# Optimization experiments

Measured on AMD Instinct MI355X. Metric: run time of the kernel, lower is better.

## Reference

```python
import jax, jax.numpy as jnp
import numpy as np
import math

B, S, H = 8, 1024, 1024
LN_EPS = 1e-5  # assumed epsilon of create_normalization_layer('layer_norm')


def setup_inputs() -> dict:
    key = jax.random.key(0)
    ks = jax.random.split(key, 6)
    context = jax.random.normal(ks[0], (B, S, H), dtype=jnp.float32)
    mask = jnp.ones((B, 1, S), dtype=jnp.int32)
    prior = jax.random.uniform(ks[1], (B, S, S), dtype=jnp.float32)
    # LayerNorm params
    gamma = jnp.ones((H,), dtype=jnp.float32)
    beta = jnp.zeros((H,), dtype=jnp.float32)
    # Dense projections (Glorot-like init)
    scale = 1.0 / np.sqrt(H)
    Wk = jax.random.normal(ks[2], (H, H), dtype=jnp.float32) * scale
    bk = jnp.zeros((H,), dtype=jnp.float32)
    Wq = jax.random.normal(ks[3], (H, H), dtype=jnp.float32) * scale
    bq = jnp.zeros((H,), dtype=jnp.float32)
    return {"context": context, "mask": mask, "prior": prior,
            "gamma": gamma, "beta": beta, "Wk": Wk, "bk": bk, "Wq": Wq, "bq": bq}


def reference(context, mask, prior, gamma, beta, Wk, bk, Wq, bq):
    dtype = context.dtype
    s = context.shape[1]
    hs = context.shape[2]
    i = jnp.arange(s)
    adj_upper = i[:, None] == (i[None, :] - 1)          # [S,S] superdiagonal
    adj_lower = i[:, None] == (i[None, :] + 1)          # subdiagonal
    adj_mask = adj_upper | adj_lower
    pad = mask[:, 0, :].astype(bool)                    # [B,S]
    pad2d = pad[:, :, None] & pad[:, None, :]           # [B,S,S]
    final_adj = adj_mask[None, :, :] & pad2d

    # LayerNorm over last axis
    mu = jnp.mean(context, axis=-1, keepdims=True)
    var = jnp.mean(jnp.square(context - mu), axis=-1, keepdims=True)
    cn = (context - mu) * jax.lax.rsqrt(var + LN_EPS) * gamma + beta

    k = cn @ Wk + bk                                    # [B,S,H]
    q = cn @ Wq + bq
    scores = jnp.einsum('bsh,bth->bst', q, k) / math.sqrt(hs)
    scores = jnp.where(final_adj, scores, jnp.asarray(-1e9, dtype))
    neibor = jax.nn.softmax(scores, axis=-1)
    neibor = jnp.sqrt(neibor * jnp.swapaxes(neibor, 1, 2) + 1e-9)
    neibor = prior + (1.0 - prior) * neibor

    triu = i[None, :] >= i[:, None]                     # [S,S] upper incl diag
    tri = triu.astype(dtype)
    b_eye = jnp.eye(s, dtype=bool)

    t = jnp.log(neibor + 1e-9)
    t = jnp.where(adj_upper[None, :, :], t, jnp.asarray(0.0, dtype))
    t = jnp.einsum('bij,jk->bik', t, tri)               # cumulative over cols
    g = jnp.exp(jnp.einsum('ij,bjk->bik', tri, t))      # hierarchical prefix product
    keep = jnp.logical_not(jnp.logical_xor(triu, b_eye))
    g = jnp.where(keep[None, :, :], g, jnp.asarray(0.0, dtype))
    neibor_diag = jnp.where(b_eye[None, :, :], jnp.asarray(1e-9, dtype), neibor)
    g = g + jnp.swapaxes(g, 1, 2) + neibor_diag
    g = g / (jnp.sum(g, axis=-1, keepdims=True) + 1e-9)

    f2d = pad2d.astype(dtype)
    g = g * f2d
    neibor = neibor * f2d
    return g, neibor
```

## Files before the change

### kernel.cpp

```cpp
#include <hip/hip_runtime.h>
#include <hip/hip_bf16.h>

#define SB 8
#define SS 1024
#define SH 1024
#define LN_EPS 1e-5f

typedef unsigned short u16;
typedef __attribute__((ext_vector_type(8))) short bf16x8;
typedef __attribute__((ext_vector_type(4))) float f32x4;

__device__ __forceinline__ u16 f2bf(float f) {
  __hip_bfloat16 h = __float2bfloat16(f);
  return *reinterpret_cast<u16*>(&h);
}
__device__ __forceinline__ float bf2f(u16 x) {
  unsigned v = ((unsigned)x) << 16;
  return __builtin_bit_cast(float, v);
}

__device__ __forceinline__ void gld16(const void* g, void* l) {
  __builtin_amdgcn_global_load_lds(
      (const __attribute__((address_space(1))) void*)g,
      (__attribute__((address_space(3))) void*)l, 16, 0, 0);
}

__global__ __launch_bounds__(256) void ln_cast(const float* __restrict__ x,
                                               const float* __restrict__ gamma,
                                               const float* __restrict__ beta,
                                               u16* __restrict__ cnb) {
  const int r = blockIdx.x;
  const int t = threadIdx.x;
  const int wave = t >> 6, lane = t & 63;
  const float* xr = x + (size_t)r * SH;
  float4 v = *(const float4*)(xr + 4 * t);

  __shared__ float p1[4], p2[4];
  float s = v.x + v.y + v.z + v.w;
#pragma unroll
  for (int off = 32; off > 0; off >>= 1) s += __shfl_down(s, off, 64);
  if (lane == 0) p1[wave] = s;
  __syncthreads();
  const float mu = (p1[0] + p1[1] + p1[2] + p1[3]) * (1.0f / SH);

  float d0 = v.x - mu, d1 = v.y - mu, d2 = v.z - mu, d3 = v.w - mu;
  float ss = d0 * d0 + d1 * d1 + d2 * d2 + d3 * d3;
#pragma unroll
  for (int off = 32; off > 0; off >>= 1) ss += __shfl_down(ss, off, 64);
  if (lane == 0) p2[wave] = ss;
  __syncthreads();
  const float rstd = rsqrtf((p2[0] + p2[1] + p2[2] + p2[3]) * (1.0f / SH) + LN_EPS);

  float4 gm = *(const float4*)(gamma + 4 * t);
  float4 bt = *(const float4*)(beta + 4 * t);
  ushort4 o;
  o.x = f2bf(d0 * rstd * gm.x + bt.x);
  o.y = f2bf(d1 * rstd * gm.y + bt.y);
  o.z = f2bf(d2 * rstd * gm.z + bt.z);
  o.w = f2bf(d3 * rstd * gm.w + bt.w);
  *(ushort4*)(cnb + (size_t)r * SH + 4 * t) = o;
}

__global__ __launch_bounds__(256) void wcast(const float* __restrict__ Wq,
                                             const float* __restrict__ Wk,
                                             u16* __restrict__ Wq_bf,
                                             u16* __restrict__ Wk_bf) {
  const size_t e = ((size_t)blockIdx.x * 256 + threadIdx.x) * 4;
  const size_t M = (size_t)SH * SH;
  const float* src;
  u16* dst;
  if (e < M) { src = Wq + e; dst = Wq_bf + e; }
  else       { src = Wk + (e - M); dst = Wk_bf + (e - M); }
  float4 v = *(const float4*)src;
  ushort4 o;
  o.x = f2bf(v.x); o.y = f2bf(v.y); o.z = f2bf(v.z); o.w = f2bf(v.w);
  *(ushort4*)dst = o;
}

__global__ __launch_bounds__(256) void wkbq_kernel(const float* __restrict__ Wk,
                                                   const float* __restrict__ bq,
                                                   float* __restrict__ wkbq) {
  const int wave = threadIdx.x >> 6, lane = threadIdx.x & 63;
  const int h = blockIdx.x * 4 + wave;
  const float* row = Wk + (size_t)h * SH;
  float s = 0.f;
#pragma unroll
  for (int v = 0; v < 4; ++v) {
    const int j = v * 256 + lane * 4;
    float4 w = *(const float4*)(row + j);
    float4 b = *(const float4*)(bq + j);
    s += w.x * b.x + w.y * b.y + w.z * b.z + w.w * b.w;
  }
#pragma unroll
  for (int off = 32; off > 0; off >>= 1) s += __shfl_down(s, off, 64);
  if (lane == 0) wkbq[h] = s;
}

#define BM 128
#define BN 128
#define BK 32

template <int GKv, int GNv, bool BF16OUT>
__global__ __launch_bounds__(256) void gemm_bt_t(const u16* __restrict__ A,
                                                 const u16* __restrict__ Bt,
                                                 void* __restrict__ Cv) {
  __shared__ u16 As[BM * BK];
  __shared__ u16 Bs[BN * BK];
  const int tid = threadIdx.x;
  const int m0 = blockIdx.y * BM;
  const int n0 = blockIdx.x * BN;
  const int wave = tid >> 6, lane = tid & 63;
  const int wm = (wave & 1) * 64, wn = (wave >> 1) * 64;
  const int l15 = lane & 15, q = lane >> 4;

  f32x4 acc[4][4] = {};

  const int srow = tid >> 2;
  const int scol = 8 * (tid & 3);
  const u16* gA = A + (size_t)(m0 + srow) * GKv + scol;
  const u16* gB = Bt + (size_t)(n0 + srow) * GKv + scol;
  u16* lA = &As[srow * BK + scol];
  u16* lB = &Bs[srow * BK + scol];

  for (int k0 = 0; k0 < GKv; k0 += BK) {
    __syncthreads();
    gld16(gA + k0, lA);
    gld16(gA + (size_t)64 * GKv + k0, lA + 64 * BK);
    gld16(gB + k0, lB);
    gld16(gB + (size_t)64 * GKv + k0, lB + 64 * BK);
    __syncthreads();

    bf16x8 af[4], bfr[4];
#pragma unroll
    for (int fm = 0; fm < 4; ++fm)
      af[fm] = *(const bf16x8*)&As[(wm + fm * 16 + l15) * BK + q * 8];
#pragma unroll
    for (int fn = 0; fn < 4; ++fn)
      bfr[fn] = *(const bf16x8*)&Bs[(wn + fn * 16 + l15) * BK + q * 8];
#pragma unroll
    for (int fm = 0; fm < 4; ++fm)
#pragma unroll
      for (int fn = 0; fn < 4; ++fn)
        acc[fm][fn] = __builtin_amdgcn_mfma_f32_16x16x32_bf16(
            af[fm], bfr[fn], acc[fm][fn], 0, 0, 0);
  }

#pragma unroll
  for (int fm = 0; fm < 4; ++fm)
#pragma unroll
    for (int fn = 0; fn < 4; ++fn) {
      const int row0 = m0 + wm + fm * 16 + q * 4;
      const int col = n0 + wn + fn * 16 + l15;
#pragma unroll
      for (int r = 0; r < 4; ++r) {
        const size_t idx = (size_t)(row0 + r) * GNv + col;
        if (BF16OUT) ((u16*)Cv)[idx] = f2bf(acc[fm][fn][r]);
        else ((float*)Cv)[idx] = acc[fm][fn][r];
      }
    }
}

__global__ __launch_bounds__(256) void adj_dots(const float* __restrict__ U,
                                                const u16* __restrict__ cnb,
                                                const float* __restrict__ wkbq,
                                                float* __restrict__ pup,
                                                float* __restrict__ pdn) {
  const int wave = threadIdx.x >> 6;
  const int lane = threadIdx.x & 63;
  const int r = blockIdx.x * 4 + wave;
  const int s = r & (SS - 1);
  const bool has_up = (s < SS - 1), has_dn = (s > 0);
  const float* ur = U + (size_t)r * SH;
  const u16* up = cnb + (size_t)(has_up ? r + 1 : r) * SH;
  const u16* dn = cnb + (size_t)(has_dn ? r - 1 : r) * SH;

  float du = 0.f, dd = 0.f;
#pragma unroll
  for (int v = 0; v < 4; ++v) {
    const int j = v * 256 + lane * 4;
    float4 uv = *(const float4*)(ur + j);
    float4 wv = *(const float4*)(wkbq + j);
    ushort4 us = *(const ushort4*)(up + j);
    ushort4 ds = *(const ushort4*)(dn + j);
    const float t0 = uv.x + wv.x, t1 = uv.y + wv.y;
    const float t2 = uv.z + wv.z, t3 = uv.w + wv.w;
    du += bf2f(us.x) * t0 + bf2f(us.y) * t1 + bf2f(us.z) * t2 + bf2f(us.w) * t3;
    dd += bf2f(ds.x) * t0 + bf2f(ds.y) * t1 + bf2f(ds.z) * t2 + bf2f(ds.w) * t3;
  }
#pragma unroll
  for (int off = 32; off > 0; off >>= 1) {
    du += __shfl_down(du, off, 64);
    dd += __shfl_down(dd, off, 64);
  }
  if (lane == 0) {
    const float scale = 0.03125f;
    du *= scale;
    dd *= scale;
    float pu, pd;
    if (!has_dn) { pu = 1.f; pd = 0.f; }
    else if (!has_up) { pu = 0.f; pd = 1.f; }
    else {
      const float m = fmaxf(du, dd);
      const float eu = __expf(du - m), ed = __expf(dd - m);
      const float inv = 1.f / (eu + ed);
      pu = eu * inv;
      pd = ed * inv;
    }
    pup[r] = pu;
    pdn[r] = pd;
  }
}

__global__ __launch_bounds__(256) void rows_kernel(const float* __restrict__ prior,
                                                   const int* __restrict__ mask,
                                                   const float* __restrict__ pup,
                                                   const float* __restrict__ pdn,
                                                   float* __restrict__ g_out,
                                                   float* __restrict__ ne_out) {
  const int r = blockIdx.x;
  const int b = r >> 10, i = r & (SS - 1);
  const int t = threadIdx.x;
  const int wave = t >> 6, lane = t & 63;
  const float nbz = 3.1622776601683795e-5f;
  const float nb_im1 = (i >= 1) ? sqrtf(pup[r - 1] * pdn[r] + 1e-9f) : nbz;
  const float nb_ip1 = (i <= SS - 2) ? sqrtf(pup[r] * pdn[r + 1] + 1e-9f) : nbz;

  const float* prow = prior + (size_t)r * SS;
  float4 pr = *(const float4*)(prow + 4 * t);
  const int* mrow = mask + b * SS;
  const float padi = (mrow[i] != 0) ? 1.f : 0.f;
  int4 mk = *(const int4*)(mrow + 4 * t);

  float ne[4], gsum = 0.f;
#pragma unroll
  for (int v = 0; v < 4; ++v) {
    const int k = 4 * t + v;
    const float p = (&pr.x)[v];
    const float nb = (k == i - 1) ? nb_im1 : (k == i + 1) ? nb_ip1 : nbz;
    const float n = p + (1.f - p) * nb;
    ne[v] = n;
    gsum += (k == i) ? (2.f + 1e-9f) : (1.f + n);
  }

  __shared__ float part[4];
#pragma unroll
  for (int off = 32; off > 0; off >>= 1) gsum += __shfl_down(gsum, off, 64);
  if (lane == 0) part[wave] = gsum;
  __syncthreads();
  const float inv = 1.f / (part[0] + part[1] + part[2] + part[3] + 1e-9f);

  float4 go, no;
#pragma unroll
  for (int v = 0; v < 4; ++v) {
    const int k = 4 * t + v;
    const float padk = ((&mk.x)[v] != 0) ? 1.f : 0.f;
    const float f2 = padi * padk;
    const float gt = (k == i) ? (2.f + 1e-9f) : (1.f + ne[v]);
    (&go.x)[v] = gt * inv * f2;
    (&no.x)[v] = ne[v] * f2;
  }
  *(float4*)(g_out + (size_t)r * SS + 4 * t) = go;
  *(float4*)(ne_out + (size_t)r * SS + 4 * t) = no;
}

extern "C" void kernel_launch(void* const* d_in, const int* in_sizes, int n_in,
                              void* d_out, int out_size, void* d_ws, size_t ws_size,
                              hipStream_t stream) {
  const float* context = (const float*)d_in[0];
  const int* mask = (const int*)d_in[1];
  const float* prior = (const float*)d_in[2];
  const float* gamma = (const float*)d_in[3];
  const float* beta = (const float*)d_in[4];
  const float* Wk = (const float*)d_in[5];
  const float* bk = (const float*)d_in[6];
  const float* Wq = (const float*)d_in[7];
  const float* bq = (const float*)d_in[8];
  (void)bk;

  float* out_g = (float*)d_out;
  float* out_n = out_g + (size_t)SB * SS * SS;

  char* ws = (char*)d_ws;
  u16* cnb = (u16*)ws;
  u16* Wq_bf = (u16*)(ws + ((size_t)16 << 20));
  u16* Wk_bf = (u16*)(ws + ((size_t)18 << 20));
  u16* PT = (u16*)(ws + ((size_t)20 << 20));
  float* U = (float*)(ws + ((size_t)24 << 20));
  float* wkbq = (float*)(ws + ((size_t)56 << 20));
  float* pup = (float*)(ws + ((size_t)57 << 20));
  float* pdn = (float*)(ws + ((size_t)57 << 20) + 8192 * sizeof(float));

  ln_cast<<<SB * SS, 256, 0, stream>>>(context, gamma, beta, cnb);
  wcast<<<2048, 256, 0, stream>>>(Wq, Wk, Wq_bf, Wk_bf);
  wkbq_kernel<<<256, 256, 0, stream>>>(Wk, bq, wkbq);
  gemm_bt_t<1024, 1024, true><<<dim3(8, 8), 256, 0, stream>>>(Wk_bf, Wq_bf, PT);
  gemm_bt_t<1024, 1024, false><<<dim3(8, 64), 256, 0, stream>>>(cnb, PT, U);
  adj_dots<<<SB * SS / 4, 256, 0, stream>>>(U, cnb, wkbq, pup, pdn);
  rows_kernel<<<SB * SS, 256, 0, stream>>>(prior, mask, pup, pdn, out_g, out_n);
}
```

Measured before the change: 209.1 us.

## Fuse neighbor dot products into U GEMM epilogue with atomic row sums

The big GEMM no longer writes the fp32 U matrix (32 MB) to memory. Its epilogue instead multiplies each accumulator by the neighboring bf16 context rows, reduces across the wave and atomically adds the result into per-row up and down sums. The bias term is split out into a separate wdot kernel, and a small softmax2 kernel finishes the two-way softmax. This removes the U write and the U re-read, at the cost of zeroing kernels, extra launches, scattered cnb loads in the epilogue and float atomics whose summation order is nondeterministic.

```diff
diff --git a/kernel.cpp b/kernel.cpp
--- a/kernel.cpp
+++ b/kernel.cpp
@@ -96,14 +96,20 @@
   if (lane == 0) wkbq[h] = s;
 }
 
+__global__ __launch_bounds__(256) void zero_f32(float* __restrict__ p) {
+  *(float4*)(p + ((size_t)blockIdx.x * 256 + threadIdx.x) * 4) =
+      make_float4(0.f, 0.f, 0.f, 0.f);
+}
+
 #define BM 128
 #define BN 128
 #define BK 32
-
-template <int GKv, int GNv, bool BF16OUT>
-__global__ __launch_bounds__(256) void gemm_bt_t(const u16* __restrict__ A,
-                                                 const u16* __restrict__ Bt,
-                                                 void* __restrict__ Cv) {
+#define GK 1024
+#define GN 1024
+
+__global__ __launch_bounds__(256) void gemm_pt(const u16* __restrict__ A,
+                                               const u16* __restrict__ Bt,
+                                               u16* __restrict__ C) {
   __shared__ u16 As[BM * BK];
   __shared__ u16 Bs[BN * BK];
   const int tid = threadIdx.x;
@@ -117,17 +123,17 @@
 
   const int srow = tid >> 2;
   const int scol = 8 * (tid & 3);
-  const u16* gA = A + (size_t)(m0 + srow) * GKv + scol;
-  const u16* gB = Bt + (size_t)(n0 + srow) * GKv + scol;
+  const u16* gA = A + (size_t)(m0 + srow) * GK + scol;
+  const u16* gB = Bt + (size_t)(n0 + srow) * GK + scol;
   u16* lA = &As[srow * BK + scol];
   u16* lB = &Bs[srow * BK + scol];
 
-  for (int k0 = 0; k0 < GKv; k0 += BK) {
+  for (int k0 = 0; k0 < GK; k0 += BK) {
     __syncthreads();
     gld16(gA + k0, lA);
-    gld16(gA + (size_t)64 * GKv + k0, lA + 64 * BK);
+    gld16(gA + (size_t)64 * GK + k0, lA + 64 * BK);
     gld16(gB + k0, lB);
-    gld16(gB + (size_t)64 * GKv + k0, lB + 64 * BK);
+    gld16(gB + (size_t)64 * GK + k0, lB + 64 * BK);
     __syncthreads();
 
     bf16x8 af[4], bfr[4];
@@ -152,63 +158,126 @@
       const int row0 = m0 + wm + fm * 16 + q * 4;
       const int col = n0 + wn + fn * 16 + l15;
 #pragma unroll
-      for (int r = 0; r < 4; ++r) {
-        const size_t idx = (size_t)(row0 + r) * GNv + col;
-        if (BF16OUT) ((u16*)Cv)[idx] = f2bf(acc[fm][fn][r]);
-        else ((float*)Cv)[idx] = acc[fm][fn][r];
+      for (int r = 0; r < 4; ++r)
+        C[(size_t)(row0 + r) * GN + col] = f2bf(acc[fm][fn][r]);
+    }
+}
+
+__global__ __launch_bounds__(256) void ugemm_fused(const u16* __restrict__ A,
+                                                   const u16* __restrict__ Bt,
+                                                   const u16* __restrict__ cnb,
+                                                   float* __restrict__ du,
+                                                   float* __restrict__ dd) {
+  __shared__ u16 As[BM * BK];
+  __shared__ u16 Bs[BN * BK];
+  const int tid = threadIdx.x;
+  const int m0 = blockIdx.y * BM;
+  const int n0 = blockIdx.x * BN;
+  const int wave = tid >> 6, lane = tid & 63;
+  const int wm = (wave & 1) * 64, wn = (wave >> 1) * 64;
+  const int l15 = lane & 15, q = lane >> 4;
+
+  f32x4 acc[4][4] = {};
+
+  const int srow = tid >> 2;
+  const int scol = 8 * (tid & 3);
+  const u16* gA = A + (size_t)(m0 + srow) * GK + scol;
+  const u16* gB = Bt + (size_t)(n0 + srow) * GK + scol;
+  u16* lA = &As[srow * BK + scol];
+  u16* lB = &Bs[srow * BK + scol];
+
+  for (int k0 = 0; k0 < GK; k0 += BK) {
+    __syncthreads();
+    gld16(gA + k0, lA);
+    gld16(gA + (size_t)64 * GK + k0, lA + 64 * BK);
+    gld16(gB + k0, lB);
+    gld16(gB + (size_t)64 * GK + k0, lB + 64 * BK);
+    __syncthreads();
+
+    bf16x8 af[4], bfr[4];
+#pragma unroll
+    for (int fm = 0; fm < 4; ++fm)
+      af[fm] = *(const bf16x8*)&As[(wm + fm * 16 + l15) * BK + q * 8];
+#pragma unroll
+    for (int fn = 0; fn < 4; ++fn)
+      bfr[fn] = *(const bf16x8*)&Bs[(wn + fn * 16 + l15) * BK + q * 8];
+#pragma unroll
+    for (int fm = 0; fm < 4; ++fm)
+#pragma unroll
+      for (int fn = 0; fn < 4; ++fn)
+        acc[fm][fn] = __builtin_amdgcn_mfma_f32_16x16x32_bf16(
+            af[fm], bfr[fn], acc[fm][fn], 0, 0, 0);
+  }
+
+#pragma unroll
+  for (int fm = 0; fm < 4; ++fm) {
+#pragma unroll
+    for (int rr = 0; rr < 4; ++rr) {
+      const int r = m0 + wm + fm * 16 + q * 4 + rr;
+      const int sl = r & (SS - 1);
+      float sdu = 0.f, sdd = 0.f;
+#pragma unroll
+      for (int fn = 0; fn < 4; ++fn) {
+        const int col = n0 + wn + fn * 16 + l15;
+        const float a = acc[fm][fn][rr];
+        if (sl < SS - 1) sdu += a * bf2f(cnb[(size_t)(r + 1) * SH + col]);
+        if (sl > 0)      sdd += a * bf2f(cnb[(size_t)(r - 1) * SH + col]);
+      }
+#pragma unroll
+      for (int m = 1; m < 16; m <<= 1) {
+        sdu += __shfl_xor(sdu, m, 64);
+        sdd += __shfl_xor(sdd, m, 64);
+      }
+      if (l15 == 0) {
+        atomicAdd(&du[r], sdu);
+        atomicAdd(&dd[r], sdd);
       }
     }
-}
-
-__global__ __launch_bounds__(256) void adj_dots(const float* __restrict__ U,
-                                                const u16* __restrict__ cnb,
-                                                const float* __restrict__ wkbq,
+  }
+}
+
+__global__ __launch_bounds__(256) void wdot(const u16* __restrict__ cnb,
+                                            const float* __restrict__ wkbq,
+                                            float* __restrict__ wvec) {
+  const int wave = threadIdx.x >> 6, lane = threadIdx.x & 63;
+  const int r = blockIdx.x * 4 + wave;
+  const u16* row = cnb + (size_t)r * SH;
+  float s = 0.f;
+#pragma unroll
+  for (int v = 0; v < 4; ++v) {
+    const int j = v * 256 + lane * 4;
+    ushort4 c = *(const ushort4*)(row + j);
+    float4 w = *(const float4*)(wkbq + j);
+    s += bf2f(c.x) * w.x + bf2f(c.y) * w.y + bf2f(c.z) * w.z + bf2f(c.w) * w.w;
+  }
+#pragma unroll
+  for (int off = 32; off > 0; off >>= 1) s += __shfl_down(s, off, 64);
+  if (lane == 0) wvec[r] = s;
+}
+
+__global__ __launch_bounds__(256) void softmax2(const float* __restrict__ du,
+                                                const float* __restrict__ dd,
+                                                const float* __restrict__ wvec,
                                                 float* __restrict__ pup,
                                                 float* __restrict__ pdn) {
-  const int wave = threadIdx.x >> 6;
-  const int lane = threadIdx.x & 63;
-  const int r = blockIdx.x * 4 + wave;
+  const int r = blockIdx.x * 256 + threadIdx.x;
   const int s = r & (SS - 1);
   const bool has_up = (s < SS - 1), has_dn = (s > 0);
-  const float* ur = U + (size_t)r * SH;
-  const u16* up = cnb + (size_t)(has_up ? r + 1 : r) * SH;
-  const u16* dn = cnb + (size_t)(has_dn ? r - 1 : r) * SH;
-
-  float du = 0.f, dd = 0.f;
-#pragma unroll
-  for (int v = 0; v < 4; ++v) {
-    const int j = v * 256 + lane * 4;
-    float4 uv = *(const float4*)(ur + j);
-    float4 wv = *(const float4*)(wkbq + j);
-    ushort4 us = *(const ushort4*)(up + j);
-    ushort4 ds = *(const ushort4*)(dn + j);
-    const float t0 = uv.x + wv.x, t1 = uv.y + wv.y;
-    const float t2 = uv.z + wv.z, t3 = uv.w + wv.w;
-    du += bf2f(us.x) * t0 + bf2f(us.y) * t1 + bf2f(us.z) * t2 + bf2f(us.w) * t3;
-    dd += bf2f(ds.x) * t0 + bf2f(ds.y) * t1 + bf2f(ds.z) * t2 + bf2f(ds.w) * t3;
-  }
-#pragma unroll
-  for (int off = 32; off > 0; off >>= 1) {
-    du += __shfl_down(du, off, 64);
-    dd += __shfl_down(dd, off, 64);
-  }
-  if (lane == 0) {
-    const float scale = 0.03125f;
-    du *= scale;
-    dd *= scale;
-    float pu, pd;
-    if (!has_dn) { pu = 1.f; pd = 0.f; }
-    else if (!has_up) { pu = 0.f; pd = 1.f; }
-    else {
-      const float m = fmaxf(du, dd);
-      const float eu = __expf(du - m), ed = __expf(dd - m);
-      const float inv = 1.f / (eu + ed);
-      pu = eu * inv;
-      pd = ed * inv;
-    }
-    pup[r] = pu;
-    pdn[r] = pd;
-  }
+  const float scale = 0.03125f;
+  float pu, pd;
+  if (!has_dn) { pu = 1.f; pd = 0.f; }
+  else if (!has_up) { pu = 0.f; pd = 1.f; }
+  else {
+    const float a = (du[r] + wvec[r + 1]) * scale;
+    const float b = (dd[r] + wvec[r - 1]) * scale;
+    const float m = fmaxf(a, b);
+    const float eu = __expf(a - m), ed = __expf(b - m);
+    const float inv = 1.f / (eu + ed);
+    pu = eu * inv;
+    pd = ed * inv;
+  }
+  pup[r] = pu;
+  pdn[r] = pd;
 }
 
 __global__ __launch_bounds__(256) void rows_kernel(const float* __restrict__ prior,
@@ -285,16 +354,21 @@
   u16* Wq_bf = (u16*)(ws + ((size_t)16 << 20));
   u16* Wk_bf = (u16*)(ws + ((size_t)18 << 20));
   u16* PT = (u16*)(ws + ((size_t)20 << 20));
-  float* U = (float*)(ws + ((size_t)24 << 20));
-  float* wkbq = (float*)(ws + ((size_t)56 << 20));
-  float* pup = (float*)(ws + ((size_t)57 << 20));
-  float* pdn = (float*)(ws + ((size_t)57 << 20) + 8192 * sizeof(float));
+  float* wkbq = (float*)(ws + ((size_t)22 << 20));
+  float* wvec = (float*)(ws + ((size_t)23 << 20));
+  float* du = (float*)(ws + ((size_t)24 << 20));
+  float* dd = (float*)(ws + ((size_t)25 << 20));
+  float* pup = (float*)(ws + ((size_t)26 << 20));
+  float* pdn = (float*)(ws + ((size_t)27 << 20));
 
   ln_cast<<<SB * SS, 256, 0, stream>>>(context, gamma, beta, cnb);
   wcast<<<2048, 256, 0, stream>>>(Wq, Wk, Wq_bf, Wk_bf);
   wkbq_kernel<<<256, 256, 0, stream>>>(Wk, bq, wkbq);
-  gemm_bt_t<1024, 1024, true><<<dim3(8, 8), 256, 0, stream>>>(Wk_bf, Wq_bf, PT);
-  gemm_bt_t<1024, 1024, false><<<dim3(8, 64), 256, 0, stream>>>(cnb, PT, U);
-  adj_dots<<<SB * SS / 4, 256, 0, stream>>>(U, cnb, wkbq, pup, pdn);
+  zero_f32<<<8, 256, 0, stream>>>(du);
+  zero_f32<<<8, 256, 0, stream>>>(dd);
+  gemm_pt<<<dim3(8, 8), 256, 0, stream>>>(Wk_bf, Wq_bf, PT);
+  ugemm_fused<<<dim3(8, 64), 256, 0, stream>>>(cnb, PT, cnb, du, dd);
+  wdot<<<SB * SS / 4, 256, 0, stream>>>(cnb, wkbq, wvec);
+  softmax2<<<SB * SS / 256, 256, 0, stream>>>(du, dd, wvec, pup, pdn);
   rows_kernel<<<SB * SS, 256, 0, stream>>>(prior, mask, pup, pdn, out_g, out_n);
 }
```

Measured after the change: 209.9 us. No clear change (+0.4%).
